# Performance work log

Measured on AMD Instinct MI355X. Metric: run time of the kernel, lower is better.

The kernel has to match this reference:

```python
import jax, jax.numpy as jnp
import numpy as np

# dummy values used when the merging vehicle does not exist (repo config constants)
DUMMY_EM_DELTA_X = 100.0
DUMMY_EM_DELTA_V = 0.0

B, T, PROJ, MERG, H = 32768, 50, 64, 3, 128
IN_DIM = PROJ + 6 + MERG  # 73


def setup_inputs() -> dict:
    key = jax.random.key(0)
    ks = jax.random.split(key, 8)
    return {
        "proj_belief": jax.random.normal(ks[0], (B, PROJ), dtype=jnp.float32),
        "idm_s": jax.random.uniform(ks[1], (B, T, 12), dtype=jnp.float32),
        "merger_cs": jax.random.normal(ks[2], (B, T, MERG), dtype=jnp.float32),
        "W1": jax.random.normal(ks[3], (IN_DIM, H), dtype=jnp.float32) * (1.0 / np.sqrt(IN_DIM)),
        "b1": jnp.zeros((H,), dtype=jnp.float32),
        "W2": jax.random.normal(ks[4], (H, H), dtype=jnp.float32) * (1.0 / np.sqrt(H)),
        "b2": jnp.zeros((H,), dtype=jnp.float32),
        "W3": jax.random.normal(ks[5], (H, 1), dtype=jnp.float32) * (1.0 / np.sqrt(H)),
        "b3": jnp.zeros((1,), dtype=jnp.float32),
        "scaler_mean": jax.random.uniform(ks[6], (6,), dtype=jnp.float32),
        "scaler_var": jax.random.uniform(ks[7], (6,), dtype=jnp.float32) + 0.5,  # positive variance
        "rollout_len": T,
    }


def reference(proj_belief, idm_s, merger_cs, W1, b1, W2, b2, W3, b3,
              scaler_mean, scaler_var, rollout_len):
    inv_std = 1.0 / jnp.sqrt(scaler_var)

    # time-major slices for scan: [T, B, F]
    idm_t = jnp.swapaxes(idm_s, 0, 1)[:rollout_len]
    merg_t = jnp.swapaxes(merger_cs, 0, 1)[:rollout_len]
    first_t = jnp.arange(rollout_len) == 0

    def step(carry, xs):
        ego_v, ego_x, act = carry  # each [B, 1]
        s, mc, first = xs          # s: [B,12], mc: [B,MERG], first: scalar bool
        f_veh_v = s[:, 1:2]
        m_veh_v = s[:, 2:3]
        f_veh_glob_x = s[:, 4:5]
        m_veh_glob_x = s[:, 5:6]
        m_veh_exists = s[:, 11:12]

        # physics update (dt = 0.1); step 0 initializes from idm_s
        ego_v = jnp.where(first, s[:, 0:1], ego_v + act * 0.1)
        ego_x = jnp.where(first, s[:, 3:4],
                          ego_x + ego_v * 0.1 + 0.5 * act * 0.1 ** 2)

        ef_delta_x = f_veh_glob_x - ego_x
        em_delta_x = (m_veh_glob_x - ego_x) * m_veh_exists \
                     + (1.0 - m_veh_exists) * DUMMY_EM_DELTA_X
        ef_dv = ego_v - f_veh_v
        em_dv = (ego_v - m_veh_v) * m_veh_exists \
                + (1.0 - m_veh_exists) * DUMMY_EM_DELTA_V

        env = jnp.concatenate([ego_v, f_veh_v, ef_dv, ef_delta_x, em_dv, em_delta_x], axis=-1)
        env = (env - scaler_mean) * inv_std

        inp = jnp.concatenate([proj_belief, env, mc], axis=-1)  # [B, 73]
        h = jax.nn.relu(inp @ W1 + b1)
        h = jax.nn.relu(h @ W2 + b2)
        act = h @ W3 + b3  # [B, 1]
        return (ego_v, ego_x, act), act

    zero = jnp.zeros((proj_belief.shape[0], 1), dtype=proj_belief.dtype)
    _, acts = jax.lax.scan(step, (zero, zero, zero), (idm_t, merg_t, first_t))
    return jnp.swapaxes(acts, 0, 1)  # [B, T, 1]
```

## Files before the change

kernel.cpp:

```cpp
#include <hip/hip_runtime.h>
#include <math.h>
#include <stdint.h>

namespace {

constexpr int T = 50;
constexpr int NB = 32768;
constexpr int H = 128;
constexpr int NTHREADS = 256;
constexpr int BLK_ROWS = 128;

typedef float v4f __attribute__((ext_vector_type(4)));
typedef float v2f __attribute__((ext_vector_type(2)));
typedef unsigned int v4u __attribute__((ext_vector_type(4)));
typedef short short8 __attribute__((ext_vector_type(8)));

union FU { float f; uint32_t u; };
union U8 { uint32_t u[4]; short8 v; };

__device__ __forceinline__ uint32_t pack_hi16(uint32_t odd, uint32_t even) {
  return (odd & 0xFFFF0000u) | (even >> 16);
}
__device__ __forceinline__ uint32_t pack_lo16(uint32_t odd, uint32_t even) {
  return (odd << 16) | (even & 0xFFFFu);
}

__device__ __forceinline__ void split2(float a, uint32_t& hi, uint32_t& mid) {
  FU c0; c0.f = a;
  uint32_t uh = c0.u & 0xFFFF0000u;
  FU fh; fh.u = uh;
  float r1 = a - fh.f;
  FU c1; c1.f = r1;
  hi = uh; mid = c1.u & 0xFFFF0000u;
}
__device__ __forceinline__ void split3(float a, uint32_t& hi, uint32_t& mid, uint32_t& lo) {
  FU c0; c0.f = a;
  uint32_t uh = c0.u & 0xFFFF0000u;
  FU fh; fh.u = uh;
  float r1 = a - fh.f;
  FU c1; c1.f = r1;
  uint32_t um = c1.u & 0xFFFF0000u;
  FU fm; fm.u = um;
  float r2 = r1 - fm.f;
  FU c2; c2.f = r2;
  hi = uh; mid = um; lo = c2.u;
}

__device__ __forceinline__ v4f mfma16(short8 a, short8 b, v4f c) {
  return __builtin_amdgcn_mfma_f32_16x16x32_bf16(a, b, c, 0, 0, 0);
}

__global__ __launch_bounds__(NTHREADS, 1)
void fwdsim4(const float* __restrict__ proj,
             const float* __restrict__ idm,
             const float* __restrict__ merg,
             const float* __restrict__ W1,
             const float* __restrict__ b1,
             const float* __restrict__ W2,
             const float* __restrict__ b2,
             const float* __restrict__ W3,
             const float* __restrict__ b3,
             const float* __restrict__ smean,
             const float* __restrict__ svar,
             float* __restrict__ out)
{
  __shared__ short8 sW1b[16 * 3 * 64];
  __shared__ short8 sEnvB[8 * 2 * 64];
  __shared__ float sBase[4 * 128 * 36];
  __shared__ uint32_t sH[4 * 32 * 36];

  const int tid  = threadIdx.x;
  const int wave = tid >> 6;
  const int lane = tid & 63;
  const int gq   = lane >> 4;
  const int o    = lane & 15;
  const int wave_row0 = blockIdx.x * BLK_ROWS + wave * 32;

  for (int job = tid; job < 1024; job += NTHREADS) {
    const int lj = job & 63, ktnt = job >> 6;
    const int k0 = (ktnt >> 3) * 32 + (lj >> 4) * 8;
    const int n  = (ktnt & 7) * 16 + (lj & 15);
    uint32_t hi[8], mi[8], lo[8];
#pragma unroll
    for (int j = 0; j < 8; ++j) split3(W1[(k0 + j) * H + n], hi[j], mi[j], lo[j]);
    U8 fh, fm, fl;
#pragma unroll
    for (int d = 0; d < 4; ++d) {
      fh.u[d] = pack_hi16(hi[2*d+1], hi[2*d]);
      fm.u[d] = pack_hi16(mi[2*d+1], mi[2*d]);
      fl.u[d] = pack_hi16(lo[2*d+1], lo[2*d]);
    }
    sW1b[(ktnt * 3 + 0) * 64 + lj] = fh.v;
    sW1b[(ktnt * 3 + 1) * 64 + lj] = fm.v;
    sW1b[(ktnt * 3 + 2) * 64 + lj] = fl.v;
  }
  for (int job = tid; job < 512; job += NTHREADS) {
    const int lj = job & 63, nt = job >> 6;
    const int k0 = (lj >> 4) * 8;
    const int n  = nt * 16 + (lj & 15);
    uint32_t hi[8], mi[8];
#pragma unroll
    for (int j = 0; j < 8; ++j) {
      const int k = k0 + j;
      const float w = (k < 9) ? W1[(64 + k) * H + n] : 0.f;
      split2(w, hi[j], mi[j]);
    }
    U8 fh, fm;
#pragma unroll
    for (int d = 0; d < 4; ++d) {
      fh.u[d] = pack_hi16(hi[2*d+1], hi[2*d]);
      fm.u[d] = pack_hi16(mi[2*d+1], mi[2*d]);
    }
    sEnvB[(nt * 2 + 0) * 64 + lj] = fh.v;
    sEnvB[(nt * 2 + 1) * 64 + lj] = fm.v;
  }

  short8 w2h[32], w2m[32];
#pragma unroll
  for (int ktnt = 0; ktnt < 32; ++ktnt) {
    const int k0 = (ktnt >> 3) * 32 + gq * 8;
    const int n  = (ktnt & 7) * 16 + o;
    uint32_t hi[8], mi[8];
#pragma unroll
    for (int j = 0; j < 8; ++j) split2(W2[(k0 + j) * H + n], hi[j], mi[j]);
    U8 fh, fm;
#pragma unroll
    for (int d = 0; d < 4; ++d) {
      fh.u[d] = pack_hi16(hi[2*d+1], hi[2*d]);
      fm.u[d] = pack_hi16(mi[2*d+1], mi[2*d]);
    }
    w2h[ktnt] = fh.v;
    w2m[ktnt] = fm.v;
  }

  float mean[6], istd[6];
#pragma unroll
  for (int c = 0; c < 6; ++c) { mean[c] = smean[c]; istd[c] = 1.0f / sqrtf(svar[c]); }
  const float b3v = b3[0];
  float b2c[8], W3c[8];
#pragma unroll
  for (int nt = 0; nt < 8; ++nt) { b2c[nt] = b2[nt*16 + o]; W3c[nt] = W3[nt*16 + o]; }

  __syncthreads();

#pragma unroll
  for (int mt = 0; mt < 2; ++mt) {
    const int row = wave_row0 + mt * 16 + o;
    short8 pah[2], pam[2], pal[2];
#pragma unroll
    for (int kt = 0; kt < 2; ++kt) {
      const float* pp = proj + (size_t)row * 64 + kt * 32 + gq * 8;
      v4f p0 = *(const v4f*)pp;
      v4f p1 = *(const v4f*)(pp + 4);
      uint32_t hi[8], mi[8], lo[8];
#pragma unroll
      for (int e = 0; e < 4; ++e) split3(p0[e], hi[e],   mi[e],   lo[e]);
#pragma unroll
      for (int e = 0; e < 4; ++e) split3(p1[e], hi[4+e], mi[4+e], lo[4+e]);
      U8 uh, um, ul;
#pragma unroll
      for (int d = 0; d < 4; ++d) {
        uh.u[d] = pack_hi16(hi[2*d+1], hi[2*d]);
        um.u[d] = pack_hi16(mi[2*d+1], mi[2*d]);
        ul.u[d] = pack_hi16(lo[2*d+1], lo[2*d]);
      }
      pah[kt] = uh.v; pam[kt] = um.v; pal[kt] = ul.v;
    }
    v4f acc[8];
#pragma unroll
    for (int nt = 0; nt < 8; ++nt) {
      const float bb = b1[nt * 16 + o];
      acc[nt] = (v4f){bb, bb, bb, bb};
    }
#pragma unroll
    for (int kt = 0; kt < 2; ++kt)
#pragma unroll
      for (int nt = 0; nt < 8; ++nt) {
        short8 bh = sW1b[((kt*8+nt)*3 + 0) * 64 + lane];
        short8 bm = sW1b[((kt*8+nt)*3 + 1) * 64 + lane];
        short8 bl = sW1b[((kt*8+nt)*3 + 2) * 64 + lane];
        acc[nt] = mfma16(pah[kt], bl, acc[nt]);
        acc[nt] = mfma16(pal[kt], bh, acc[nt]);
        acc[nt] = mfma16(pam[kt], bm, acc[nt]);
        acc[nt] = mfma16(pah[kt], bm, acc[nt]);
        acc[nt] = mfma16(pam[kt], bh, acc[nt]);
        acc[nt] = mfma16(pah[kt], bh, acc[nt]);
      }
#pragma unroll
    for (int nt = 0; nt < 8; ++nt) {
      float* dst = &sBase[(wave * 128 + nt*16 + o) * 36 + mt*16 + 4*gq];
      *(v4f*)dst = acc[nt];
    }
  }

  float ego_v[2], ego_x[2], act[2] = {0.f, 0.f};
  const float* idmp[2] = { idm + (size_t)(wave_row0 + o) * (T*12),
                           idm + (size_t)(wave_row0 + 16 + o) * (T*12) };
  const float* mrgp[2] = { merg + (size_t)(wave_row0 + o) * (T*3),
                           merg + (size_t)(wave_row0 + 16 + o) * (T*3) };
  v4f sa[2]; v2f fb[2]; float exr[2], m0[2], m1[2], m2[2];
  v4f nsa[2]; v2f nfb[2]; float nex[2], nm0[2], nm1[2], nm2[2];
#pragma unroll
  for (int mt = 0; mt < 2; ++mt) {
    sa[mt] = *(const v4f*)idmp[mt];
    fb[mt] = *(const v2f*)(idmp[mt] + 4);
    exr[mt] = idmp[mt][11];
    m0[mt] = mrgp[mt][0]; m1[mt] = mrgp[mt][1]; m2[mt] = mrgp[mt][2];
  }

#pragma unroll 1
  for (int t = 0; t < T; ++t) {
    float xk[2][9];
#pragma unroll
    for (int mt = 0; mt < 2; ++mt) {
      const float s0 = sa[mt][0], fv = sa[mt][1], mv = sa[mt][2], s3 = sa[mt][3];
      const float fgx = fb[mt][0], mgx = fb[mt][1];
      const float ex = exr[mt];
      if (t == 0) { ego_v[mt] = s0; ego_x[mt] = s3; }
      else {
        ego_v[mt] += act[mt] * 0.1f;
        ego_x[mt] += ego_v[mt] * 0.1f + act[mt] * 0.005f;
      }
      xk[mt][0] = (ego_v[mt]                                      - mean[0]) * istd[0];
      xk[mt][1] = (fv                                             - mean[1]) * istd[1];
      xk[mt][2] = (ego_v[mt] - fv                                 - mean[2]) * istd[2];
      xk[mt][3] = (fgx - ego_x[mt]                                - mean[3]) * istd[3];
      xk[mt][4] = ((ego_v[mt] - mv) * ex                          - mean[4]) * istd[4];
      xk[mt][5] = ((mgx - ego_x[mt]) * ex + (1.0f - ex) * 100.0f  - mean[5]) * istd[5];
      xk[mt][6] = m0[mt]; xk[mt][7] = m1[mt]; xk[mt][8] = m2[mt];
    }
    if (t + 1 < T) {
#pragma unroll
      for (int mt = 0; mt < 2; ++mt) {
        const float* ip = idmp[mt] + (t + 1) * 12;
        nsa[mt] = *(const v4f*)ip;  nfb[mt] = *(const v2f*)(ip + 4);  nex[mt] = ip[11];
        const float* mp = mrgp[mt] + (t + 1) * 3;
        nm0[mt] = mp[0]; nm1[mt] = mp[1]; nm2[mt] = mp[2];
      }
    }

    short8 eh[2], em[2];
#pragma unroll
    for (int mt = 0; mt < 2; ++mt) {
      uint32_t hi[8], mi[8];
#pragma unroll
      for (int j = 0; j < 8; ++j) {
        float v = (gq == 0) ? xk[mt][j] : ((gq == 1 && j == 0) ? xk[mt][8] : 0.f);
        split2(v, hi[j], mi[j]);
      }
      U8 uh, um;
#pragma unroll
      for (int d = 0; d < 4; ++d) {
        uh.u[d] = pack_hi16(hi[2*d+1], hi[2*d]);
        um.u[d] = pack_hi16(mi[2*d+1], mi[2*d]);
      }
      eh[mt] = uh.v; em[mt] = um.v;
    }

    v4f acc2[2][8];
#pragma unroll
    for (int mt = 0; mt < 2; ++mt)
#pragma unroll
      for (int nt = 0; nt < 8; ++nt)
        acc2[mt][nt] = (v4f){b2c[nt], b2c[nt], b2c[nt], b2c[nt]};

#pragma unroll
    for (int kt = 0; kt < 4; ++kt) {
#pragma unroll
      for (int mt = 0; mt < 2; ++mt)
#pragma unroll
        for (int ntl = 0; ntl < 2; ++ntl) {
          const int nt = kt * 2 + ntl;
          v4f a1 = *(const v4f*)&sBase[(wave*128 + nt*16 + o) * 36 + mt*16 + 4*gq];
          short8 bh = sEnvB[(nt*2 + 0) * 64 + lane];
          short8 bm = sEnvB[(nt*2 + 1) * 64 + lane];
          a1 = mfma16(eh[mt], bm, a1);
          a1 = mfma16(em[mt], bh, a1);
          a1 = mfma16(eh[mt], bh, a1);
#pragma unroll
          for (int r = 0; r < 4; ++r) {
            const float hv = fmaxf(a1[r], 0.f);
            uint32_t hi, mi; split2(hv, hi, mi);
            sH[(wave*32 + mt*16 + 4*gq + r) * 36 + ntl*16 + o] = hi | (mi >> 16);
          }
        }
#pragma unroll
      for (int mt = 0; mt < 2; ++mt) {
        const uint32_t* src = &sH[(wave*32 + mt*16 + o) * 36 + gq*8];
        v4u q0 = *(const v4u*)src;
        v4u q1 = *(const v4u*)(src + 4);
        uint32_t u[8] = {q0[0], q0[1], q0[2], q0[3], q1[0], q1[1], q1[2], q1[3]};
        U8 uh, um;
#pragma unroll
        for (int d = 0; d < 4; ++d) {
          uh.u[d] = pack_hi16(u[2*d+1], u[2*d]);
          um.u[d] = pack_lo16(u[2*d+1], u[2*d]);
        }
        short8 ah = uh.v, am = um.v;
#pragma unroll
        for (int nt = 0; nt < 8; ++nt) {
          acc2[mt][nt] = mfma16(ah, w2m[kt*8 + nt], acc2[mt][nt]);
          acc2[mt][nt] = mfma16(am, w2h[kt*8 + nt], acc2[mt][nt]);
          acc2[mt][nt] = mfma16(ah, w2h[kt*8 + nt], acc2[mt][nt]);
        }
      }
    }

    float part[2][4];
#pragma unroll
    for (int mt = 0; mt < 2; ++mt)
#pragma unroll
      for (int r = 0; r < 4; ++r) part[mt][r] = 0.f;
#pragma unroll
    for (int mt = 0; mt < 2; ++mt)
#pragma unroll
      for (int nt = 0; nt < 8; ++nt) {
        v4f h = acc2[mt][nt];
#pragma unroll
        for (int r = 0; r < 4; ++r) part[mt][r] += fmaxf(h[r], 0.f) * W3c[nt];
      }
#pragma unroll
    for (int m = 1; m <= 8; m <<= 1)
#pragma unroll
      for (int mt = 0; mt < 2; ++mt)
#pragma unroll
        for (int r = 0; r < 4; ++r) part[mt][r] += __shfl_xor(part[mt][r], m, 64);

    const int src = ((o >> 2) << 4) | o;
#pragma unroll
    for (int mt = 0; mt < 2; ++mt) {
      const float c0 = __shfl(part[mt][0], src, 64);
      const float c1 = __shfl(part[mt][1], src, 64);
      const float c2 = __shfl(part[mt][2], src, 64);
      const float c3 = __shfl(part[mt][3], src, 64);
      const float slo = (o & 1) ? c1 : c0;
      const float shi = (o & 1) ? c3 : c2;
      act[mt] = ((o & 2) ? shi : slo) + b3v;
    }

    if (gq == 0) {
      out[(size_t)(wave_row0 + o)      * T + t] = act[0];
      out[(size_t)(wave_row0 + 16 + o) * T + t] = act[1];
    }

#pragma unroll
    for (int mt = 0; mt < 2; ++mt) {
      sa[mt] = nsa[mt]; fb[mt] = nfb[mt]; exr[mt] = nex[mt];
      m0[mt] = nm0[mt]; m1[mt] = nm1[mt]; m2[mt] = nm2[mt];
    }
  }
}

}

extern "C" void kernel_launch(void* const* d_in, const int* in_sizes, int n_in,
                              void* d_out, int out_size, void* d_ws, size_t ws_size,
                              hipStream_t stream) {
  const float* proj  = (const float*)d_in[0];
  const float* idm   = (const float*)d_in[1];
  const float* merg  = (const float*)d_in[2];
  const float* W1    = (const float*)d_in[3];
  const float* b1    = (const float*)d_in[4];
  const float* W2    = (const float*)d_in[5];
  const float* b2    = (const float*)d_in[6];
  const float* W3    = (const float*)d_in[7];
  const float* b3    = (const float*)d_in[8];
  const float* smean = (const float*)d_in[9];
  const float* svar  = (const float*)d_in[10];

  dim3 grid(NB / BLK_ROWS);
  dim3 block(NTHREADS);
  hipLaunchKernelGGL(fwdsim4, grid, block, 0, stream,
                     proj, idm, merg, W1, b1, W2, b2, W3, b3, smean, svar,
                     (float*)d_out);
}
```

Baseline: 437.1 us.

## Split hidden dimension across waves so each block handles 32 rows

Each block now processes 32 rows instead of 128, with each of the four waves owning 32 of the 128 hidden units instead of all units for its own rows. W1 and W2 slices are held in registers, so the LDS-staged weights and per-wave base buffer go away. Layer-2 inputs are shared through LDS with a block barrier each step, and the final dot product is reduced with DPP row sums plus a cross-wave LDS sum. The next-step input prefetch is dropped. This cuts register pressure (launch bounds raised to 2 blocks per CU) and quadruples the grid, at the cost of two __syncthreads per timestep and redundant recomputation of the env features in every wave.

After: 451.0 us. +3.2%, slower.

```diff
diff --git a/kernel.cpp b/kernel.cpp
--- a/kernel.cpp
+++ b/kernel.cpp
@@ -8,7 +8,7 @@
 constexpr int NB = 32768;
 constexpr int H = 128;
 constexpr int NTHREADS = 256;
-constexpr int BLK_ROWS = 128;
+constexpr int BLK_ROWS = 32;
 
 typedef float v4f __attribute__((ext_vector_type(4)));
 typedef float v2f __attribute__((ext_vector_type(2)));
@@ -50,8 +50,30 @@
   return __builtin_amdgcn_mfma_f32_16x16x32_bf16(a, b, c, 0, 0, 0);
 }
 
-__global__ __launch_bounds__(NTHREADS, 1)
-void fwdsim4(const float* __restrict__ proj,
+__device__ __forceinline__ short8 pack8(const uint32_t* w) {
+  U8 f;
+#pragma unroll
+  for (int d = 0; d < 4; ++d) f.u[d] = pack_hi16(w[2*d+1], w[2*d]);
+  return f.v;
+}
+
+template <int CTRL>
+__device__ __forceinline__ float ror_add(float x) {
+  FU a; a.f = x;
+  int r = __builtin_amdgcn_update_dpp(0, (int)a.u, CTRL, 0xF, 0xF, false);
+  FU b; b.u = (uint32_t)r;
+  return x + b.f;
+}
+__device__ __forceinline__ float row_sum16(float x) {
+  x = ror_add<0x128>(x);
+  x = ror_add<0x124>(x);
+  x = ror_add<0x122>(x);
+  x = ror_add<0x121>(x);
+  return x;
+}
+
+__global__ __launch_bounds__(NTHREADS, 2)
+void fwdsim5(const float* __restrict__ proj,
              const float* __restrict__ idm,
              const float* __restrict__ merg,
              const float* __restrict__ W1,
@@ -64,92 +86,75 @@
              const float* __restrict__ svar,
              float* __restrict__ out)
 {
-  __shared__ short8 sW1b[16 * 3 * 64];
-  __shared__ short8 sEnvB[8 * 2 * 64];
-  __shared__ float sBase[4 * 128 * 36];
-  __shared__ uint32_t sH[4 * 32 * 36];
+  __shared__ uint32_t sHc[32 * 132];
+  __shared__ float actP[32 * 4];
 
   const int tid  = threadIdx.x;
   const int wave = tid >> 6;
   const int lane = tid & 63;
   const int gq   = lane >> 4;
   const int o    = lane & 15;
-  const int wave_row0 = blockIdx.x * BLK_ROWS + wave * 32;
-
-  for (int job = tid; job < 1024; job += NTHREADS) {
-    const int lj = job & 63, ktnt = job >> 6;
-    const int k0 = (ktnt >> 3) * 32 + (lj >> 4) * 8;
-    const int n  = (ktnt & 7) * 16 + (lj & 15);
-    uint32_t hi[8], mi[8], lo[8];
-#pragma unroll
-    for (int j = 0; j < 8; ++j) split3(W1[(k0 + j) * H + n], hi[j], mi[j], lo[j]);
-    U8 fh, fm, fl;
-#pragma unroll
-    for (int d = 0; d < 4; ++d) {
-      fh.u[d] = pack_hi16(hi[2*d+1], hi[2*d]);
-      fm.u[d] = pack_hi16(mi[2*d+1], mi[2*d]);
-      fl.u[d] = pack_hi16(lo[2*d+1], lo[2*d]);
-    }
-    sW1b[(ktnt * 3 + 0) * 64 + lj] = fh.v;
-    sW1b[(ktnt * 3 + 1) * 64 + lj] = fm.v;
-    sW1b[(ktnt * 3 + 2) * 64 + lj] = fl.v;
-  }
-  for (int job = tid; job < 512; job += NTHREADS) {
-    const int lj = job & 63, nt = job >> 6;
-    const int k0 = (lj >> 4) * 8;
-    const int n  = nt * 16 + (lj & 15);
+  const int row0 = blockIdx.x * BLK_ROWS;
+
+  const int n0 = wave * 32 + o;
+  const int n1 = n0 + 16;
+
+  float mean[6], istd[6];
+#pragma unroll
+  for (int c = 0; c < 6; ++c) { mean[c] = smean[c]; istd[c] = 1.0f / sqrtf(svar[c]); }
+  const float b3v  = b3[0];
+  const float b2c0 = b2[n0], b2c1 = b2[n1];
+  const float w3c0 = W3[n0], w3c1 = W3[n1];
+
+  short8 envh[2], envm[2];
+#pragma unroll
+  for (int ntl = 0; ntl < 2; ++ntl) {
+    const int n = ntl ? n1 : n0;
     uint32_t hi[8], mi[8];
 #pragma unroll
     for (int j = 0; j < 8; ++j) {
-      const int k = k0 + j;
+      const int k = gq * 8 + j;
       const float w = (k < 9) ? W1[(64 + k) * H + n] : 0.f;
       split2(w, hi[j], mi[j]);
     }
-    U8 fh, fm;
-#pragma unroll
-    for (int d = 0; d < 4; ++d) {
-      fh.u[d] = pack_hi16(hi[2*d+1], hi[2*d]);
-      fm.u[d] = pack_hi16(mi[2*d+1], mi[2*d]);
-    }
-    sEnvB[(nt * 2 + 0) * 64 + lj] = fh.v;
-    sEnvB[(nt * 2 + 1) * 64 + lj] = fm.v;
+    envh[ntl] = pack8(hi);
+    envm[ntl] = pack8(mi);
   }
 
-  short8 w2h[32], w2m[32];
-#pragma unroll
-  for (int ktnt = 0; ktnt < 32; ++ktnt) {
-    const int k0 = (ktnt >> 3) * 32 + gq * 8;
-    const int n  = (ktnt & 7) * 16 + o;
-    uint32_t hi[8], mi[8];
-#pragma unroll
-    for (int j = 0; j < 8; ++j) split2(W2[(k0 + j) * H + n], hi[j], mi[j]);
-    U8 fh, fm;
-#pragma unroll
-    for (int d = 0; d < 4; ++d) {
-      fh.u[d] = pack_hi16(hi[2*d+1], hi[2*d]);
-      fm.u[d] = pack_hi16(mi[2*d+1], mi[2*d]);
-    }
-    w2h[ktnt] = fh.v;
-    w2m[ktnt] = fm.v;
+  short8 w2h[8], w2m[8];
+#pragma unroll
+  for (int kt = 0; kt < 4; ++kt)
+#pragma unroll
+    for (int ntl = 0; ntl < 2; ++ntl) {
+      const int n = ntl ? n1 : n0;
+      uint32_t hi[8], mi[8];
+#pragma unroll
+      for (int j = 0; j < 8; ++j) split2(W2[(kt * 32 + gq * 8 + j) * H + n], hi[j], mi[j]);
+      w2h[kt * 2 + ntl] = pack8(hi);
+      w2m[kt * 2 + ntl] = pack8(mi);
+    }
+
+  v4f base[2][2];
+#pragma unroll
+  for (int mt = 0; mt < 2; ++mt) {
+    base[mt][0] = (v4f){b2c0 * 0.f + b1[n0], b1[n0], b1[n0], b1[n0]};
+    base[mt][1] = (v4f){b1[n1], b1[n1], b1[n1], b1[n1]};
+    base[mt][0][0] = b1[n0];
   }
-
-  float mean[6], istd[6];
-#pragma unroll
-  for (int c = 0; c < 6; ++c) { mean[c] = smean[c]; istd[c] = 1.0f / sqrtf(svar[c]); }
-  const float b3v = b3[0];
-  float b2c[8], W3c[8];
-#pragma unroll
-  for (int nt = 0; nt < 8; ++nt) { b2c[nt] = b2[nt*16 + o]; W3c[nt] = W3[nt*16 + o]; }
-
-  __syncthreads();
-
-#pragma unroll
-  for (int mt = 0; mt < 2; ++mt) {
-    const int row = wave_row0 + mt * 16 + o;
-    short8 pah[2], pam[2], pal[2];
-#pragma unroll
-    for (int kt = 0; kt < 2; ++kt) {
-      const float* pp = proj + (size_t)row * 64 + kt * 32 + gq * 8;
+#pragma unroll
+  for (int kt2 = 0; kt2 < 2; ++kt2) {
+    short8 bh[2], bm[2], bl[2];
+#pragma unroll
+    for (int ntl = 0; ntl < 2; ++ntl) {
+      const int n = ntl ? n1 : n0;
+      uint32_t hi[8], mi[8], lo[8];
+#pragma unroll
+      for (int j = 0; j < 8; ++j) split3(W1[(kt2 * 32 + gq * 8 + j) * H + n], hi[j], mi[j], lo[j]);
+      bh[ntl] = pack8(hi); bm[ntl] = pack8(mi); bl[ntl] = pack8(lo);
+    }
+#pragma unroll
+    for (int mt = 0; mt < 2; ++mt) {
+      const float* pp = proj + (size_t)(row0 + mt * 16 + o) * 64 + kt2 * 32 + gq * 8;
       v4f p0 = *(const v4f*)pp;
       v4f p1 = *(const v4f*)(pp + 4);
       uint32_t hi[8], mi[8], lo[8];
@@ -157,86 +162,49 @@
       for (int e = 0; e < 4; ++e) split3(p0[e], hi[e],   mi[e],   lo[e]);
 #pragma unroll
       for (int e = 0; e < 4; ++e) split3(p1[e], hi[4+e], mi[4+e], lo[4+e]);
-      U8 uh, um, ul;
-#pragma unroll
-      for (int d = 0; d < 4; ++d) {
-        uh.u[d] = pack_hi16(hi[2*d+1], hi[2*d]);
-        um.u[d] = pack_hi16(mi[2*d+1], mi[2*d]);
-        ul.u[d] = pack_hi16(lo[2*d+1], lo[2*d]);
-      }
-      pah[kt] = uh.v; pam[kt] = um.v; pal[kt] = ul.v;
-    }
-    v4f acc[8];
-#pragma unroll
-    for (int nt = 0; nt < 8; ++nt) {
-      const float bb = b1[nt * 16 + o];
-      acc[nt] = (v4f){bb, bb, bb, bb};
-    }
-#pragma unroll
-    for (int kt = 0; kt < 2; ++kt)
-#pragma unroll
-      for (int nt = 0; nt < 8; ++nt) {
-        short8 bh = sW1b[((kt*8+nt)*3 + 0) * 64 + lane];
-        short8 bm = sW1b[((kt*8+nt)*3 + 1) * 64 + lane];
-        short8 bl = sW1b[((kt*8+nt)*3 + 2) * 64 + lane];
-        acc[nt] = mfma16(pah[kt], bl, acc[nt]);
-        acc[nt] = mfma16(pal[kt], bh, acc[nt]);
-        acc[nt] = mfma16(pam[kt], bm, acc[nt]);
-        acc[nt] = mfma16(pah[kt], bm, acc[nt]);
-        acc[nt] = mfma16(pam[kt], bh, acc[nt]);
-        acc[nt] = mfma16(pah[kt], bh, acc[nt]);
-      }
-#pragma unroll
-    for (int nt = 0; nt < 8; ++nt) {
-      float* dst = &sBase[(wave * 128 + nt*16 + o) * 36 + mt*16 + 4*gq];
-      *(v4f*)dst = acc[nt];
+      short8 pah = pack8(hi), pam = pack8(mi), pal = pack8(lo);
+#pragma unroll
+      for (int ntl = 0; ntl < 2; ++ntl) {
+        v4f a = base[mt][ntl];
+        a = mfma16(pah, bl[ntl], a);
+        a = mfma16(pal, bh[ntl], a);
+        a = mfma16(pam, bm[ntl], a);
+        a = mfma16(pah, bm[ntl], a);
+        a = mfma16(pam, bh[ntl], a);
+        a = mfma16(pah, bh[ntl], a);
+        base[mt][ntl] = a;
+      }
     }
   }
 
+  const float* idmp[2] = { idm + (size_t)(row0 + o) * (T * 12),
+                           idm + (size_t)(row0 + 16 + o) * (T * 12) };
+  const float* mrgp[2] = { merg + (size_t)(row0 + o) * (T * 3),
+                           merg + (size_t)(row0 + 16 + o) * (T * 3) };
   float ego_v[2], ego_x[2], act[2] = {0.f, 0.f};
-  const float* idmp[2] = { idm + (size_t)(wave_row0 + o) * (T*12),
-                           idm + (size_t)(wave_row0 + 16 + o) * (T*12) };
-  const float* mrgp[2] = { merg + (size_t)(wave_row0 + o) * (T*3),
-                           merg + (size_t)(wave_row0 + 16 + o) * (T*3) };
-  v4f sa[2]; v2f fb[2]; float exr[2], m0[2], m1[2], m2[2];
-  v4f nsa[2]; v2f nfb[2]; float nex[2], nm0[2], nm1[2], nm2[2];
-#pragma unroll
-  for (int mt = 0; mt < 2; ++mt) {
-    sa[mt] = *(const v4f*)idmp[mt];
-    fb[mt] = *(const v2f*)(idmp[mt] + 4);
-    exr[mt] = idmp[mt][11];
-    m0[mt] = mrgp[mt][0]; m1[mt] = mrgp[mt][1]; m2[mt] = mrgp[mt][2];
-  }
 
 #pragma unroll 1
   for (int t = 0; t < T; ++t) {
     float xk[2][9];
 #pragma unroll
     for (int mt = 0; mt < 2; ++mt) {
-      const float s0 = sa[mt][0], fv = sa[mt][1], mv = sa[mt][2], s3 = sa[mt][3];
-      const float fgx = fb[mt][0], mgx = fb[mt][1];
-      const float ex = exr[mt];
-      if (t == 0) { ego_v[mt] = s0; ego_x[mt] = s3; }
+      const float* ip = idmp[mt] + t * 12;
+      v4f s = *(const v4f*)ip;
+      v2f f = *(const v2f*)(ip + 4);
+      const float ex = ip[11];
+      const float* mp = mrgp[mt] + t * 3;
+      if (t == 0) { ego_v[mt] = s[0]; ego_x[mt] = s[3]; }
       else {
         ego_v[mt] += act[mt] * 0.1f;
         ego_x[mt] += ego_v[mt] * 0.1f + act[mt] * 0.005f;
       }
-      xk[mt][0] = (ego_v[mt]                                      - mean[0]) * istd[0];
-      xk[mt][1] = (fv                                             - mean[1]) * istd[1];
-      xk[mt][2] = (ego_v[mt] - fv                                 - mean[2]) * istd[2];
-      xk[mt][3] = (fgx - ego_x[mt]                                - mean[3]) * istd[3];
-      xk[mt][4] = ((ego_v[mt] - mv) * ex                          - mean[4]) * istd[4];
-      xk[mt][5] = ((mgx - ego_x[mt]) * ex + (1.0f - ex) * 100.0f  - mean[5]) * istd[5];
-      xk[mt][6] = m0[mt]; xk[mt][7] = m1[mt]; xk[mt][8] = m2[mt];
-    }
-    if (t + 1 < T) {
-#pragma unroll
-      for (int mt = 0; mt < 2; ++mt) {
-        const float* ip = idmp[mt] + (t + 1) * 12;
-        nsa[mt] = *(const v4f*)ip;  nfb[mt] = *(const v2f*)(ip + 4);  nex[mt] = ip[11];
-        const float* mp = mrgp[mt] + (t + 1) * 3;
-        nm0[mt] = mp[0]; nm1[mt] = mp[1]; nm2[mt] = mp[2];
-      }
+      xk[mt][0] = (ego_v[mt]                                     - mean[0]) * istd[0];
+      xk[mt][1] = (s[1]                                          - mean[1]) * istd[1];
+      xk[mt][2] = (ego_v[mt] - s[1]                              - mean[2]) * istd[2];
+      xk[mt][3] = (f[0] - ego_x[mt]                              - mean[3]) * istd[3];
+      xk[mt][4] = ((ego_v[mt] - s[2]) * ex                       - mean[4]) * istd[4];
+      xk[mt][5] = ((f[1] - ego_x[mt]) * ex + (1.0f - ex) * 100.f - mean[5]) * istd[5];
+      xk[mt][6] = mp[0]; xk[mt][7] = mp[1]; xk[mt][8] = mp[2];
     }
 
     short8 eh[2], em[2];
@@ -245,48 +213,41 @@
       uint32_t hi[8], mi[8];
 #pragma unroll
       for (int j = 0; j < 8; ++j) {
-        float v = (gq == 0) ? xk[mt][j] : ((gq == 1 && j == 0) ? xk[mt][8] : 0.f);
+        const float v = (gq == 0) ? xk[mt][j] : ((gq == 1 && j == 0) ? xk[mt][8] : 0.f);
         split2(v, hi[j], mi[j]);
       }
-      U8 uh, um;
-#pragma unroll
-      for (int d = 0; d < 4; ++d) {
-        uh.u[d] = pack_hi16(hi[2*d+1], hi[2*d]);
-        um.u[d] = pack_hi16(mi[2*d+1], mi[2*d]);
-      }
-      eh[mt] = uh.v; em[mt] = um.v;
-    }
-
-    v4f acc2[2][8];
+      eh[mt] = pack8(hi);
+      em[mt] = pack8(mi);
+    }
+
 #pragma unroll
     for (int mt = 0; mt < 2; ++mt)
 #pragma unroll
-      for (int nt = 0; nt < 8; ++nt)
-        acc2[mt][nt] = (v4f){b2c[nt], b2c[nt], b2c[nt], b2c[nt]};
-
-#pragma unroll
-    for (int kt = 0; kt < 4; ++kt) {
-#pragma unroll
-      for (int mt = 0; mt < 2; ++mt)
-#pragma unroll
-        for (int ntl = 0; ntl < 2; ++ntl) {
-          const int nt = kt * 2 + ntl;
-          v4f a1 = *(const v4f*)&sBase[(wave*128 + nt*16 + o) * 36 + mt*16 + 4*gq];
-          short8 bh = sEnvB[(nt*2 + 0) * 64 + lane];
-          short8 bm = sEnvB[(nt*2 + 1) * 64 + lane];
-          a1 = mfma16(eh[mt], bm, a1);
-          a1 = mfma16(em[mt], bh, a1);
-          a1 = mfma16(eh[mt], bh, a1);
-#pragma unroll
-          for (int r = 0; r < 4; ++r) {
-            const float hv = fmaxf(a1[r], 0.f);
-            uint32_t hi, mi; split2(hv, hi, mi);
-            sH[(wave*32 + mt*16 + 4*gq + r) * 36 + ntl*16 + o] = hi | (mi >> 16);
-          }
+      for (int ntl = 0; ntl < 2; ++ntl) {
+        v4f a1 = base[mt][ntl];
+        a1 = mfma16(eh[mt], envm[ntl], a1);
+        a1 = mfma16(em[mt], envh[ntl], a1);
+        a1 = mfma16(eh[mt], envh[ntl], a1);
+#pragma unroll
+        for (int r = 0; r < 4; ++r) {
+          const float hv = fmaxf(a1[r], 0.f);
+          uint32_t hi, mi; split2(hv, hi, mi);
+          sHc[(mt * 16 + 4 * gq + r) * 132 + wave * 32 + ntl * 16 + o] = hi | (mi >> 16);
         }
-#pragma unroll
-      for (int mt = 0; mt < 2; ++mt) {
-        const uint32_t* src = &sH[(wave*32 + mt*16 + o) * 36 + gq*8];
+      }
+    __syncthreads();
+
+    v4f acc[2][2];
+#pragma unroll
+    for (int mt = 0; mt < 2; ++mt) {
+      acc[mt][0] = (v4f){b2c0, b2c0, b2c0, b2c0};
+      acc[mt][1] = (v4f){b2c1, b2c1, b2c1, b2c1};
+    }
+#pragma unroll
+    for (int mt = 0; mt < 2; ++mt)
+#pragma unroll
+      for (int kt = 0; kt < 4; ++kt) {
+        const uint32_t* src = &sHc[(mt * 16 + o) * 132 + kt * 32 + gq * 8];
         v4u q0 = *(const v4u*)src;
         v4u q1 = *(const v4u*)(src + 4);
         uint32_t u[8] = {q0[0], q0[1], q0[2], q0[3], q1[0], q1[1], q1[2], q1[3]};
@@ -296,57 +257,42 @@
           uh.u[d] = pack_hi16(u[2*d+1], u[2*d]);
           um.u[d] = pack_lo16(u[2*d+1], u[2*d]);
         }
-        short8 ah = uh.v, am = um.v;
-#pragma unroll
-        for (int nt = 0; nt < 8; ++nt) {
-          acc2[mt][nt] = mfma16(ah, w2m[kt*8 + nt], acc2[mt][nt]);
-          acc2[mt][nt] = mfma16(am, w2h[kt*8 + nt], acc2[mt][nt]);
-          acc2[mt][nt] = mfma16(ah, w2h[kt*8 + nt], acc2[mt][nt]);
+        const short8 ah = uh.v, am = um.v;
+#pragma unroll
+        for (int ntl = 0; ntl < 2; ++ntl) {
+          v4f a = acc[mt][ntl];
+          a = mfma16(ah, w2m[kt * 2 + ntl], a);
+          a = mfma16(am, w2h[kt * 2 + ntl], a);
+          a = mfma16(ah, w2h[kt * 2 + ntl], a);
+          acc[mt][ntl] = a;
         }
       }
-    }
-
-    float part[2][4];
-#pragma unroll
-    for (int mt = 0; mt < 2; ++mt)
-#pragma unroll
-      for (int r = 0; r < 4; ++r) part[mt][r] = 0.f;
-#pragma unroll
-    for (int mt = 0; mt < 2; ++mt)
-#pragma unroll
-      for (int nt = 0; nt < 8; ++nt) {
-        v4f h = acc2[mt][nt];
-#pragma unroll
-        for (int r = 0; r < 4; ++r) part[mt][r] += fmaxf(h[r], 0.f) * W3c[nt];
-      }
-#pragma unroll
-    for (int m = 1; m <= 8; m <<= 1)
-#pragma unroll
-      for (int mt = 0; mt < 2; ++mt)
-#pragma unroll
-        for (int r = 0; r < 4; ++r) part[mt][r] += __shfl_xor(part[mt][r], m, 64);
-
-    const int src = ((o >> 2) << 4) | o;
-#pragma unroll
-    for (int mt = 0; mt < 2; ++mt) {
-      const float c0 = __shfl(part[mt][0], src, 64);
-      const float c1 = __shfl(part[mt][1], src, 64);
-      const float c2 = __shfl(part[mt][2], src, 64);
-      const float c3 = __shfl(part[mt][3], src, 64);
-      const float slo = (o & 1) ? c1 : c0;
-      const float shi = (o & 1) ? c3 : c2;
-      act[mt] = ((o & 2) ? shi : slo) + b3v;
-    }
-
-    if (gq == 0) {
-      out[(size_t)(wave_row0 + o)      * T + t] = act[0];
-      out[(size_t)(wave_row0 + 16 + o) * T + t] = act[1];
-    }
-
-#pragma unroll
-    for (int mt = 0; mt < 2; ++mt) {
-      sa[mt] = nsa[mt]; fb[mt] = nfb[mt]; exr[mt] = nex[mt];
-      m0[mt] = nm0[mt]; m1[mt] = nm1[mt]; m2[mt] = nm2[mt];
+
+#pragma unroll
+    for (int mt = 0; mt < 2; ++mt) {
+      float part[4];
+#pragma unroll
+      for (int r = 0; r < 4; ++r)
+        part[r] = fmaxf(acc[mt][0][r], 0.f) * w3c0 + fmaxf(acc[mt][1][r], 0.f) * w3c1;
+#pragma unroll
+      for (int r = 0; r < 4; ++r) part[r] = row_sum16(part[r]);
+      if (o == 0) {
+#pragma unroll
+        for (int r = 0; r < 4; ++r)
+          actP[(mt * 16 + 4 * gq + r) * 4 + wave] = part[r];
+      }
+    }
+    __syncthreads();
+
+#pragma unroll
+    for (int mt = 0; mt < 2; ++mt) {
+      v4f ap = *(const v4f*)&actP[(mt * 16 + o) * 4];
+      act[mt] = ap[0] + ap[1] + ap[2] + ap[3] + b3v;
+    }
+
+    if (wave == 0 && gq == 0) {
+      out[(size_t)(row0 + o)      * T + t] = act[0];
+      out[(size_t)(row0 + 16 + o) * T + t] = act[1];
     }
   }
 }
@@ -370,7 +316,7 @@
 
   dim3 grid(NB / BLK_ROWS);
   dim3 block(NTHREADS);
-  hipLaunchKernelGGL(fwdsim4, grid, block, 0, stream,
+  hipLaunchKernelGGL(fwdsim5, grid, block, 0, stream,
                      proj, idm, merg, W1, b1, W2, b2, W3, b3, smean, svar,
                      (float*)d_out);
 }
```
